# Optimization experiments

Measured on AMD Instinct MI355X. Metric: run time of the kernel, lower is better.

The kernel has to match this reference:

```python
import jax, jax.numpy as jnp
import numpy as np

IN_F, OUT_F = 64, 32
N = IN_F * OUT_F + OUT_F  # 2080 sampled parameters (weights + bias)
B, S = 8, 2048
SCALE_INIT = 1.0 * float(np.sqrt(2.0 / (IN_F + OUT_F)))


def setup_inputs() -> dict:
    key = jax.random.key(0)
    k_x, k_eps, k_loc, k_cov = jax.random.split(key, 4)
    x = jax.random.normal(k_x, (B, S, IN_F), dtype=jnp.float32)
    eps = jax.random.normal(k_eps, (B, S, N), dtype=jnp.float32)
    loc = 0.01 * jax.random.normal(k_loc, (N,), dtype=jnp.float32)
    logvar = jnp.full((N,), float(np.log(SCALE_INIT)), dtype=jnp.float32)
    n_off = N * (N - 1) // 2
    cov_flat = 0.001 * jax.random.normal(k_cov, (n_off,), dtype=jnp.float32)
    return {"x": x, "eps": eps, "loc": loc, "logvar": logvar, "cov_flat": cov_flat}


def reference(x, eps, loc, logvar, cov_flat):
    n = loc.shape[0]
    in_f = x.shape[-1]
    out_f = n // (in_f + 1)  # n = out*(in+1)
    # flat_to_triangular (strictly lower) + make_cholesky, vectorized scatter
    rows, cols = np.tril_indices(n, -1)
    A = jnp.zeros((n, n), dtype=x.dtype).at[rows, cols].set(cov_flat)
    L = A + jnp.diag(jnp.exp(logvar * 0.5))  # off-diag from cov, diag = std
    # MultivariateNormal rsample: loc + L @ eps (per batch sample)
    W = loc + jnp.einsum('bsn,mn->bsm', eps, L)  # [B,S,N]
    b = W[..., :out_f]
    Wm = W[..., out_f:].reshape(*W.shape[:-1], in_f, out_f)  # [B,S,in,out]
    y = jnp.einsum('bsh,bshk->bsk', x, Wm) + b
    return y
```

## Files before the change

### kernel.cpp

```cpp
#include <hip/hip_runtime.h>
#include <hip/hip_bf16.h>

#define IN_F  64
#define OUT_F 32
#define NV    2080
#define NPAD  2176
#define MM    16384
#define KK    2080
#define NBN   17

typedef __attribute__((ext_vector_type(4))) float f32x4;
typedef __bf16 bf16x8 __attribute__((ext_vector_type(8)));

using gas_ptr = const __attribute__((address_space(1))) void*;
using lds_ptr = __attribute__((address_space(3))) void*;

__global__ __launch_bounds__(256) void build_L_k(const float* __restrict__ cov,
                                                 const float* __restrict__ logvar,
                                                 __hip_bfloat16* __restrict__ LB) {
    const int idx = blockIdx.x * 256 + threadIdx.x;
    const int m = idx / KK;
    const int k = idx - m * KK;
    float v = 0.0f;
    if (m < NV) {
        if (k < m)       v = cov[(size_t)(m * (m - 1) / 2) + k];
        else if (k == m) v = expf(0.5f * logvar[m]);
    }
    LB[idx] = __float2bfloat16(v);
}

__global__ __launch_bounds__(256) void gemm_zl_k(const float* __restrict__ A,
                                                 const __hip_bfloat16* __restrict__ BT,
                                                 const float* __restrict__ loc,
                                                 const float* __restrict__ x,
                                                 float* __restrict__ Ypart) {
    __shared__ __align__(16) __hip_bfloat16 As[2][128 * 32];
    __shared__ __align__(16) __hip_bfloat16 Bs[2][128 * 32];
    __shared__ float xs[128][4];

    const int tid  = threadIdx.x;
    const int bm   = blockIdx.x;
    const int bn   = (NBN - 1) - blockIdx.y;
    const int wave = tid >> 6;
    const int lane = tid & 63;
    const int quad = lane >> 4;
    const int r16  = lane & 15;

    const int kblocks = min(KK / 32, 4 * bn + 4);

    {
        const int tl = tid >> 1;
        const int cc = (tid & 1) * 2;
#pragma unroll
        for (int c = cc; c < cc + 2; c++) {
            const int h = 4 * bn - 1 + c;
            float w = 0.0f;
            if (bn == 0 && c == 0)          w = 1.0f;
            else if (h >= 0 && h < IN_F)    w = x[(size_t)(bm * 128 + tl) * IN_F + h];
            xs[tl][c] = w;
        }
    }

    const float*          Ag = A  + (size_t)bm * 128 * KK;
    const __hip_bfloat16* Bg = BT + (size_t)bn * 128 * KK;

    const int c0 = tid, c1 = tid + 256;
    const int ar0 = c0 >> 2, ap0 = (c0 & 3) ^ ((ar0 >> 1) & 3);
    const int ar1 = c1 >> 2, ap1 = (c1 & 3) ^ ((ar1 >> 1) & 3);
    const size_t gofs0 = (size_t)ar0 * KK + ap0 * 8;
    const size_t gofs1 = (size_t)ar1 * KK + ap1 * 8;

    f32x4 acc[2][8];
#pragma unroll
    for (int i = 0; i < 2; i++)
#pragma unroll
        for (int j = 0; j < 8; j++) acc[i][j] = f32x4{0.f, 0.f, 0.f, 0.f};

    int aofs[2], bofs[8];
#pragma unroll
    for (int i = 0; i < 2; i++) {
        const int arow = 32 * wave + 16 * i + r16;
        aofs[i] = arow * 32 + (quad ^ ((arow >> 1) & 3)) * 8;
    }
#pragma unroll
    for (int j = 0; j < 8; j++) {
        const int brow = 16 * j + r16;
        bofs[j] = brow * 32 + (quad ^ ((brow >> 1) & 3)) * 8;
    }

    {
        f32x4 ra0 = *(const f32x4*)(Ag + gofs0);
        f32x4 ra1 = *(const f32x4*)(Ag + gofs0 + 4);
        f32x4 ra2 = *(const f32x4*)(Ag + gofs1);
        f32x4 ra3 = *(const f32x4*)(Ag + gofs1 + 4);
        __builtin_amdgcn_global_load_lds((gas_ptr)(Bg + gofs0), (lds_ptr)(&Bs[0][0] + c0 * 8), 16, 0, 0);
        __builtin_amdgcn_global_load_lds((gas_ptr)(Bg + gofs1), (lds_ptr)(&Bs[0][0] + c1 * 8), 16, 0, 0);
        bf16x8 w0, w1;
#pragma unroll
        for (int q = 0; q < 4; q++) {
            w0[q] = (__bf16)ra0[q]; w0[4 + q] = (__bf16)ra1[q];
            w1[q] = (__bf16)ra2[q]; w1[4 + q] = (__bf16)ra3[q];
        }
        *(bf16x8*)(&As[0][0] + c0 * 8) = w0;
        *(bf16x8*)(&As[0][0] + c1 * 8) = w1;
    }

    for (int kb = 0; kb < kblocks; ++kb) {
        const int cur = kb & 1;
        __syncthreads();

        const bool pf = (kb + 1 < kblocks);
        f32x4 ra0, ra1, ra2, ra3;
        if (pf) {
            const size_t k0 = (size_t)(kb + 1) * 32;
            ra0 = *(const f32x4*)(Ag + k0 + gofs0);
            ra1 = *(const f32x4*)(Ag + k0 + gofs0 + 4);
            ra2 = *(const f32x4*)(Ag + k0 + gofs1);
            ra3 = *(const f32x4*)(Ag + k0 + gofs1 + 4);
            __builtin_amdgcn_global_load_lds((gas_ptr)(Bg + k0 + gofs0), (lds_ptr)(&Bs[cur ^ 1][0] + c0 * 8), 16, 0, 0);
            __builtin_amdgcn_global_load_lds((gas_ptr)(Bg + k0 + gofs1), (lds_ptr)(&Bs[cur ^ 1][0] + c1 * 8), 16, 0, 0);
        }

        bf16x8 af[2], bfr[8];
#pragma unroll
        for (int i = 0; i < 2; i++) af[i]  = *(const bf16x8*)(&As[cur][0] + aofs[i]);
#pragma unroll
        for (int j = 0; j < 8; j++) bfr[j] = *(const bf16x8*)(&Bs[cur][0] + bofs[j]);
#pragma unroll
        for (int i = 0; i < 2; i++)
#pragma unroll
            for (int j = 0; j < 8; j++)
                acc[i][j] = __builtin_amdgcn_mfma_f32_16x16x32_bf16(af[i], bfr[j], acc[i][j], 0, 0, 0);

        if (pf) {
            bf16x8 w0, w1;
#pragma unroll
            for (int q = 0; q < 4; q++) {
                w0[q] = (__bf16)ra0[q]; w0[4 + q] = (__bf16)ra1[q];
                w1[q] = (__bf16)ra2[q]; w1[4 + q] = (__bf16)ra3[q];
            }
            *(bf16x8*)(&As[cur ^ 1][0] + c0 * 8) = w0;
            *(bf16x8*)(&As[cur ^ 1][0] + c1 * 8) = w1;
        }
    }

    float locv[8];
#pragma unroll
    for (int j = 0; j < 8; j++) {
        const int col = bn * 128 + 16 * j + r16;
        locv[j] = (col < NV) ? loc[col] : 0.0f;
    }

    float* yp = Ypart + ((size_t)bn * MM + (size_t)bm * 128) * OUT_F;
#pragma unroll
    for (int i = 0; i < 2; i++) {
#pragma unroll
        for (int r = 0; r < 4; r++) {
            const int tl = 32 * wave + 16 * i + 4 * quad + r;
            float v0 = 0.0f, v1 = 0.0f;
#pragma unroll
            for (int c = 0; c < 4; c++) {
                const float w = xs[tl][c];
                v0 += w * (acc[i][2 * c][r]     + locv[2 * c]);
                v1 += w * (acc[i][2 * c + 1][r] + locv[2 * c + 1]);
            }
            yp[(size_t)tl * OUT_F + r16]      = v0;
            yp[(size_t)tl * OUT_F + 16 + r16] = v1;
        }
    }
}

__global__ __launch_bounds__(256) void reduce_y_k(const float4* __restrict__ yp,
                                                  float4* __restrict__ y) {
    const size_t i = (size_t)blockIdx.x * 256 + threadIdx.x;
    float4 s = yp[i];
#pragma unroll
    for (int b = 1; b < NBN; b++) {
        float4 v = yp[i + (size_t)b * (MM * OUT_F / 4)];
        s.x += v.x; s.y += v.y; s.z += v.z; s.w += v.w;
    }
    y[i] = s;
}

extern "C" void kernel_launch(void* const* d_in, const int* in_sizes, int n_in,
                              void* d_out, int out_size, void* d_ws, size_t ws_size,
                              hipStream_t stream) {
    const float* x      = (const float*)d_in[0];
    const float* eps    = (const float*)d_in[1];
    const float* loc    = (const float*)d_in[2];
    const float* logvar = (const float*)d_in[3];
    const float* cov    = (const float*)d_in[4];
    float* y = (float*)d_out;

    char* ws = (char*)d_ws;
    __hip_bfloat16* LB    = (__hip_bfloat16*)ws;
    float*          Ypart = (float*)(ws + (size_t)NPAD * KK * 2);

    build_L_k<<<(NPAD * KK) / 256, 256, 0, stream>>>(cov, logvar, LB);
    gemm_zl_k<<<dim3(MM / 128, NBN), 256, 0, stream>>>(eps, LB, loc, x, Ypart);
    reduce_y_k<<<(MM * OUT_F / 4) / 256, 256, 0, stream>>>((const float4*)Ypart, (float4*)y);
}
```

Measured before the change: 314.5 us.

## Pre-convert eps to bf16 and use triple-buffered async GEMM with 256-row tiles

A fused prep kernel converts eps to bf16 in workspace while also building L. The GEMM then streams both operands with direct global-to-LDS loads into a three-stage buffer, uses 256-row M tiles (each wave computes 4x8 MFMA tiles), and skips MFMAs on the zero upper-triangular part of L in the diagonal blocks. This removes the in-loop fp32-to-bf16 conversion and register staging of A and raises data reuse per tile. The cost is an extra full pass over eps (read fp32, write bf16, read again) plus more LDS and register use. The old path stays as a fallback when the workspace is too small.

```diff
diff --git a/kernel.cpp b/kernel.cpp
--- a/kernel.cpp
+++ b/kernel.cpp
@@ -8,12 +8,43 @@
 #define MM    16384
 #define KK    2080
 #define NBN   17
+#define BM    256
+
+#define CVT_BLKS 16640
+#define L_BLKS   17680
 
 typedef __attribute__((ext_vector_type(4))) float f32x4;
 typedef __bf16 bf16x8 __attribute__((ext_vector_type(8)));
 
 using gas_ptr = const __attribute__((address_space(1))) void*;
 using lds_ptr = __attribute__((address_space(3))) void*;
+
+__global__ __launch_bounds__(256) void prep_k(const float* __restrict__ eps,
+                                              const float* __restrict__ cov,
+                                              const float* __restrict__ logvar,
+                                              __hip_bfloat16* __restrict__ EB,
+                                              __hip_bfloat16* __restrict__ LB) {
+    const int b = blockIdx.x;
+    if (b < CVT_BLKS) {
+        const size_t i = ((size_t)b * 256 + threadIdx.x) * 8;
+        const f32x4 a0 = *(const f32x4*)(eps + i);
+        const f32x4 a1 = *(const f32x4*)(eps + i + 4);
+        bf16x8 w;
+#pragma unroll
+        for (int q = 0; q < 4; q++) { w[q] = (__bf16)a0[q]; w[4 + q] = (__bf16)a1[q]; }
+        *(bf16x8*)(EB + i) = w;
+    } else {
+        const int idx = (b - CVT_BLKS) * 256 + threadIdx.x;
+        const int m = idx / KK;
+        const int k = idx - m * KK;
+        float v = 0.0f;
+        if (m < NV) {
+            if (k < m)       v = cov[(size_t)(m * (m - 1) / 2) + k];
+            else if (k == m) v = expf(0.5f * logvar[m]);
+        }
+        LB[idx] = __float2bfloat16(v);
+    }
+}
 
 __global__ __launch_bounds__(256) void build_L_k(const float* __restrict__ cov,
                                                  const float* __restrict__ logvar,
@@ -29,6 +60,151 @@
     LB[idx] = __float2bfloat16(v);
 }
 
+__global__ __launch_bounds__(256, 2) void gemm_v2_k(const __hip_bfloat16* __restrict__ EB,
+                                                    const __hip_bfloat16* __restrict__ LBt,
+                                                    const float* __restrict__ loc,
+                                                    const float* __restrict__ x,
+                                                    float* __restrict__ Ypart) {
+    __shared__ __align__(16) __hip_bfloat16 As[3][BM * 32];
+    __shared__ __align__(16) __hip_bfloat16 Bs[3][128 * 32];
+    __shared__ float xs[BM][4];
+
+    const int tid  = threadIdx.x;
+    const int bm   = blockIdx.x;
+    const int bn   = (NBN - 1) - blockIdx.y;
+    const int wave = tid >> 6;
+    const int lane = tid & 63;
+    const int quad = lane >> 4;
+    const int r16  = lane & 15;
+    const int kblocks = min(KK / 32, 4 * bn + 4);
+
+    {
+        const int row = bm * BM + tid;
+#pragma unroll
+        for (int c = 0; c < 4; c++) {
+            const int h = 4 * bn - 1 + c;
+            float w = 0.0f;
+            if (bn == 0 && c == 0)       w = 1.0f;
+            else if (h >= 0 && h < IN_F) w = x[(size_t)row * IN_F + h];
+            xs[tid][c] = w;
+        }
+    }
+
+    const __hip_bfloat16* __restrict__ Ag = EB  + (size_t)bm * BM * KK;
+    const __hip_bfloat16* __restrict__ Bg = LBt + (size_t)bn * 128 * KK;
+
+    size_t agofs[4]; int aldso[4];
+#pragma unroll
+    for (int u = 0; u < 4; u++) {
+        const int c = tid + 256 * u;
+        const int r = c >> 2, p = (c & 3) ^ ((r >> 1) & 3);
+        agofs[u] = (size_t)r * KK + (size_t)(p * 8);
+        aldso[u] = c * 8;
+    }
+    size_t bgofs[2]; int bldso[2];
+#pragma unroll
+    for (int u = 0; u < 2; u++) {
+        const int c = tid + 256 * u;
+        const int r = c >> 2, p = (c & 3) ^ ((r >> 1) & 3);
+        bgofs[u] = (size_t)r * KK + (size_t)(p * 8);
+        bldso[u] = c * 8;
+    }
+
+    int aofs[4], bofs[8];
+#pragma unroll
+    for (int i = 0; i < 4; i++) {
+        const int arow = 64 * wave + 16 * i + r16;
+        aofs[i] = arow * 32 + (quad ^ ((arow >> 1) & 3)) * 8;
+    }
+#pragma unroll
+    for (int j = 0; j < 8; j++) {
+        const int brow = 16 * j + r16;
+        bofs[j] = brow * 32 + (quad ^ ((brow >> 1) & 3)) * 8;
+    }
+
+    f32x4 acc[4][8];
+#pragma unroll
+    for (int i = 0; i < 4; i++)
+#pragma unroll
+        for (int j = 0; j < 8; j++) acc[i][j] = f32x4{0.f, 0.f, 0.f, 0.f};
+
+    auto stage = [&](int t, int buf) __attribute__((always_inline)) {
+        const size_t k0 = (size_t)t * 32;
+#pragma unroll
+        for (int u = 0; u < 4; u++)
+            __builtin_amdgcn_global_load_lds((gas_ptr)(Ag + k0 + agofs[u]),
+                                             (lds_ptr)(&As[buf][0] + aldso[u]), 16, 0, 0);
+#pragma unroll
+        for (int u = 0; u < 2; u++)
+            __builtin_amdgcn_global_load_lds((gas_ptr)(Bg + k0 + bgofs[u]),
+                                             (lds_ptr)(&Bs[buf][0] + bldso[u]), 16, 0, 0);
+    };
+
+    stage(0, 0);
+    stage(1, 1);
+    asm volatile("s_waitcnt lgkmcnt(0)" ::: "memory");
+    asm volatile("s_waitcnt vmcnt(6)" ::: "memory");
+    __builtin_amdgcn_s_barrier();
+    __builtin_amdgcn_sched_barrier(0);
+
+    auto iter = [&](int t, int jlo) __attribute__((always_inline)) {
+        if (t + 2 < kblocks) stage(t + 2, (t + 2) % 3);
+        const __hip_bfloat16* as = &As[t % 3][0];
+        const __hip_bfloat16* bs = &Bs[t % 3][0];
+        bf16x8 af[4], bfr[8];
+#pragma unroll
+        for (int i = 0; i < 4; i++) af[i] = *(const bf16x8*)(as + aofs[i]);
+#pragma unroll
+        for (int j = 0; j < 8; j++)
+            if (j >= jlo) bfr[j] = *(const bf16x8*)(bs + bofs[j]);
+#pragma unroll
+        for (int j = 0; j < 8; j++)
+            if (j >= jlo)
+#pragma unroll
+                for (int i = 0; i < 4; i++)
+                    acc[i][j] = __builtin_amdgcn_mfma_f32_16x16x32_bf16(af[i], bfr[j], acc[i][j], 0, 0, 0);
+        if (t + 2 < kblocks) {
+            asm volatile("s_waitcnt vmcnt(6)" ::: "memory");
+            __builtin_amdgcn_s_barrier();
+            __builtin_amdgcn_sched_barrier(0);
+        } else if (t + 1 < kblocks) {
+            asm volatile("s_waitcnt vmcnt(0)" ::: "memory");
+            __builtin_amdgcn_s_barrier();
+            __builtin_amdgcn_sched_barrier(0);
+        }
+    };
+
+    const int t_full = min(kblocks, 4 * bn + 1);
+    int t = 0;
+    for (; t < t_full; ++t) iter(t, 0);
+    for (; t < kblocks; ++t) iter(t, 2 * t - 8 * bn);
+
+    float locv[8];
+#pragma unroll
+    for (int j = 0; j < 8; j++) {
+        const int col = bn * 128 + 16 * j + r16;
+        locv[j] = (col < NV) ? loc[col] : 0.0f;
+    }
+
+    float* yp = Ypart + ((size_t)bn * MM + (size_t)bm * BM) * OUT_F;
+#pragma unroll
+    for (int i = 0; i < 4; i++) {
+#pragma unroll
+        for (int r = 0; r < 4; r++) {
+            const int tl = 64 * wave + 16 * i + 4 * quad + r;
+            float v0 = 0.0f, v1 = 0.0f;
+#pragma unroll
+            for (int c = 0; c < 4; c++) {
+                const float w = xs[tl][c];
+                v0 += w * (acc[i][2 * c][r]     + locv[2 * c]);
+                v1 += w * (acc[i][2 * c + 1][r] + locv[2 * c + 1]);
+            }
+            yp[(size_t)tl * OUT_F + r16]      = v0;
+            yp[(size_t)tl * OUT_F + 16 + r16] = v1;
+        }
+    }
+}
+
 __global__ __launch_bounds__(256) void gemm_zl_k(const float* __restrict__ A,
                                                  const __hip_bfloat16* __restrict__ BT,
                                                  const float* __restrict__ loc,
@@ -193,10 +369,24 @@
     float* y = (float*)d_out;
 
     char* ws = (char*)d_ws;
-    __hip_bfloat16* LB    = (__hip_bfloat16*)ws;
-    float*          Ypart = (float*)(ws + (size_t)NPAD * KK * 2);
-
-    build_L_k<<<(NPAD * KK) / 256, 256, 0, stream>>>(cov, logvar, LB);
-    gemm_zl_k<<<dim3(MM / 128, NBN), 256, 0, stream>>>(eps, LB, loc, x, Ypart);
-    reduce_y_k<<<(MM * OUT_F / 4) / 256, 256, 0, stream>>>((const float4*)Ypart, (float4*)y);
-}
+    const size_t lb_bytes = (size_t)NPAD * KK * 2;
+    const size_t eb_bytes = (size_t)MM * KK * 2;
+    const size_t yp_bytes = (size_t)NBN * MM * OUT_F * 4;
+
+    if (ws_size >= lb_bytes + eb_bytes + yp_bytes) {
+        __hip_bfloat16* LB    = (__hip_bfloat16*)ws;
+        __hip_bfloat16* EB    = (__hip_bfloat16*)(ws + lb_bytes);
+        float*          Ypart = (float*)(ws + lb_bytes + eb_bytes);
+
+        prep_k<<<CVT_BLKS + L_BLKS, 256, 0, stream>>>(eps, cov, logvar, EB, LB);
+        gemm_v2_k<<<dim3(MM / BM, NBN), 256, 0, stream>>>(EB, LB, loc, x, Ypart);
+        reduce_y_k<<<(MM * OUT_F / 4) / 256, 256, 0, stream>>>((const float4*)Ypart, (float4*)y);
+    } else {
+        __hip_bfloat16* LB    = (__hip_bfloat16*)ws;
+        float*          Ypart = (float*)(ws + lb_bytes);
+
+        build_L_k<<<(NPAD * KK) / 256, 256, 0, stream>>>(cov, logvar, LB);
+        gemm_zl_k<<<dim3(MM / 128, NBN), 256, 0, stream>>>(eps, LB, loc, x, Ypart);
+        reduce_y_k<<<(MM * OUT_F / 4) / 256, 256, 0, stream>>>((const float4*)Ypart, (float4*)y);
+    }
+}
```

Measured after the change: 325.4 us. +3.4%, slower.

## Enlarge GEMM M-tile to 256, triple-buffer B, skip zero triangular MFMAs

Applied to the files above, without the earlier changes.

The GEMM tile grows from 128 to 256 rows per block, so each B (L-transposed) tile loaded into LDS is reused across twice as many eps rows. B staging becomes a three-stage async pipeline with explicit waitcnt and barrier control, plus MFMA priority raising. In the diagonal k-blocks, MFMAs for column fragments whose L entries are all zero (upper triangle) are skipped. The larger tile halves the grid and raises register pressure (acc is now 4x8 f32x4), which could reduce occupancy despite the launch_bounds hint.

```diff
diff --git a/kernel.cpp b/kernel.cpp
--- a/kernel.cpp
+++ b/kernel.cpp
@@ -8,6 +8,7 @@
 #define MM    16384
 #define KK    2080
 #define NBN   17
+#define BM    256
 
 typedef __attribute__((ext_vector_type(4))) float f32x4;
 typedef __bf16 bf16x8 __attribute__((ext_vector_type(8)));
@@ -29,14 +30,14 @@
     LB[idx] = __float2bfloat16(v);
 }
 
-__global__ __launch_bounds__(256) void gemm_zl_k(const float* __restrict__ A,
-                                                 const __hip_bfloat16* __restrict__ BT,
-                                                 const float* __restrict__ loc,
-                                                 const float* __restrict__ x,
-                                                 float* __restrict__ Ypart) {
-    __shared__ __align__(16) __hip_bfloat16 As[2][128 * 32];
-    __shared__ __align__(16) __hip_bfloat16 Bs[2][128 * 32];
-    __shared__ float xs[128][4];
+__global__ __launch_bounds__(256, 2) void gemm_v3_k(const float* __restrict__ A,
+                                                    const __hip_bfloat16* __restrict__ BT,
+                                                    const float* __restrict__ loc,
+                                                    const float* __restrict__ x,
+                                                    float* __restrict__ Ypart) {
+    __shared__ __align__(16) __hip_bfloat16 As[2][BM * 32];
+    __shared__ __align__(16) __hip_bfloat16 Bs[3][128 * 32];
+    __shared__ float xs[BM][4];
 
     const int tid  = threadIdx.x;
     const int bm   = blockIdx.x;
@@ -45,41 +46,44 @@
     const int lane = tid & 63;
     const int quad = lane >> 4;
     const int r16  = lane & 15;
-
     const int kblocks = min(KK / 32, 4 * bn + 4);
 
     {
-        const int tl = tid >> 1;
-        const int cc = (tid & 1) * 2;
-#pragma unroll
-        for (int c = cc; c < cc + 2; c++) {
+        const int row = bm * BM + tid;
+#pragma unroll
+        for (int c = 0; c < 4; c++) {
             const int h = 4 * bn - 1 + c;
             float w = 0.0f;
-            if (bn == 0 && c == 0)          w = 1.0f;
-            else if (h >= 0 && h < IN_F)    w = x[(size_t)(bm * 128 + tl) * IN_F + h];
-            xs[tl][c] = w;
-        }
-    }
-
-    const float*          Ag = A  + (size_t)bm * 128 * KK;
-    const __hip_bfloat16* Bg = BT + (size_t)bn * 128 * KK;
-
-    const int c0 = tid, c1 = tid + 256;
-    const int ar0 = c0 >> 2, ap0 = (c0 & 3) ^ ((ar0 >> 1) & 3);
-    const int ar1 = c1 >> 2, ap1 = (c1 & 3) ^ ((ar1 >> 1) & 3);
-    const size_t gofs0 = (size_t)ar0 * KK + ap0 * 8;
-    const size_t gofs1 = (size_t)ar1 * KK + ap1 * 8;
-
-    f32x4 acc[2][8];
-#pragma unroll
-    for (int i = 0; i < 2; i++)
-#pragma unroll
-        for (int j = 0; j < 8; j++) acc[i][j] = f32x4{0.f, 0.f, 0.f, 0.f};
-
-    int aofs[2], bofs[8];
-#pragma unroll
-    for (int i = 0; i < 2; i++) {
-        const int arow = 32 * wave + 16 * i + r16;
+            if (bn == 0 && c == 0)       w = 1.0f;
+            else if (h >= 0 && h < IN_F) w = x[(size_t)row * IN_F + h];
+            xs[tid][c] = w;
+        }
+    }
+
+    const float*          __restrict__ Ag = A  + (size_t)bm * BM * KK;
+    const __hip_bfloat16* __restrict__ Bg = BT + (size_t)bn * 128 * KK;
+
+    size_t agofs[4]; int aldso[4];
+#pragma unroll
+    for (int u = 0; u < 4; u++) {
+        const int c = tid + 256 * u;
+        const int r = c >> 2, p = (c & 3) ^ ((r >> 1) & 3);
+        agofs[u] = (size_t)r * KK + (size_t)(p * 8);
+        aldso[u] = c * 8;
+    }
+    size_t bgofs[2]; int bldso[2];
+#pragma unroll
+    for (int u = 0; u < 2; u++) {
+        const int c = tid + 256 * u;
+        const int r = c >> 2, p = (c & 3) ^ ((r >> 1) & 3);
+        bgofs[u] = (size_t)r * KK + (size_t)(p * 8);
+        bldso[u] = c * 8;
+    }
+
+    int aofs[4], bofs[8];
+#pragma unroll
+    for (int i = 0; i < 4; i++) {
+        const int arow = 64 * wave + 16 * i + r16;
         aofs[i] = arow * 32 + (quad ^ ((arow >> 1) & 3)) * 8;
     }
 #pragma unroll
@@ -88,61 +92,90 @@
         bofs[j] = brow * 32 + (quad ^ ((brow >> 1) & 3)) * 8;
     }
 
-    {
-        f32x4 ra0 = *(const f32x4*)(Ag + gofs0);
-        f32x4 ra1 = *(const f32x4*)(Ag + gofs0 + 4);
-        f32x4 ra2 = *(const f32x4*)(Ag + gofs1);
-        f32x4 ra3 = *(const f32x4*)(Ag + gofs1 + 4);
-        __builtin_amdgcn_global_load_lds((gas_ptr)(Bg + gofs0), (lds_ptr)(&Bs[0][0] + c0 * 8), 16, 0, 0);
-        __builtin_amdgcn_global_load_lds((gas_ptr)(Bg + gofs1), (lds_ptr)(&Bs[0][0] + c1 * 8), 16, 0, 0);
-        bf16x8 w0, w1;
-#pragma unroll
-        for (int q = 0; q < 4; q++) {
-            w0[q] = (__bf16)ra0[q]; w0[4 + q] = (__bf16)ra1[q];
-            w1[q] = (__bf16)ra2[q]; w1[4 + q] = (__bf16)ra3[q];
-        }
-        *(bf16x8*)(&As[0][0] + c0 * 8) = w0;
-        *(bf16x8*)(&As[0][0] + c1 * 8) = w1;
-    }
-
-    for (int kb = 0; kb < kblocks; ++kb) {
-        const int cur = kb & 1;
-        __syncthreads();
-
-        const bool pf = (kb + 1 < kblocks);
-        f32x4 ra0, ra1, ra2, ra3;
-        if (pf) {
-            const size_t k0 = (size_t)(kb + 1) * 32;
-            ra0 = *(const f32x4*)(Ag + k0 + gofs0);
-            ra1 = *(const f32x4*)(Ag + k0 + gofs0 + 4);
-            ra2 = *(const f32x4*)(Ag + k0 + gofs1);
-            ra3 = *(const f32x4*)(Ag + k0 + gofs1 + 4);
-            __builtin_amdgcn_global_load_lds((gas_ptr)(Bg + k0 + gofs0), (lds_ptr)(&Bs[cur ^ 1][0] + c0 * 8), 16, 0, 0);
-            __builtin_amdgcn_global_load_lds((gas_ptr)(Bg + k0 + gofs1), (lds_ptr)(&Bs[cur ^ 1][0] + c1 * 8), 16, 0, 0);
-        }
-
-        bf16x8 af[2], bfr[8];
-#pragma unroll
-        for (int i = 0; i < 2; i++) af[i]  = *(const bf16x8*)(&As[cur][0] + aofs[i]);
-#pragma unroll
-        for (int j = 0; j < 8; j++) bfr[j] = *(const bf16x8*)(&Bs[cur][0] + bofs[j]);
-#pragma unroll
-        for (int i = 0; i < 2; i++)
-#pragma unroll
-            for (int j = 0; j < 8; j++)
-                acc[i][j] = __builtin_amdgcn_mfma_f32_16x16x32_bf16(af[i], bfr[j], acc[i][j], 0, 0, 0);
-
-        if (pf) {
-            bf16x8 w0, w1;
+    f32x4 acc[4][8];
+#pragma unroll
+    for (int i = 0; i < 4; i++)
+#pragma unroll
+        for (int j = 0; j < 8; j++) acc[i][j] = f32x4{0.f, 0.f, 0.f, 0.f};
+
+    f32x4 ra[8];
+
+    auto loadA = [&](int t) __attribute__((always_inline)) {
+        const size_t k0 = (size_t)t * 32;
+#pragma unroll
+        for (int u = 0; u < 4; u++) {
+            ra[2 * u]     = *(const f32x4*)(Ag + k0 + agofs[u]);
+            ra[2 * u + 1] = *(const f32x4*)(Ag + k0 + agofs[u] + 4);
+        }
+    };
+    auto writeA = [&](int buf) __attribute__((always_inline)) {
+#pragma unroll
+        for (int u = 0; u < 4; u++) {
+            bf16x8 w;
 #pragma unroll
             for (int q = 0; q < 4; q++) {
-                w0[q] = (__bf16)ra0[q]; w0[4 + q] = (__bf16)ra1[q];
-                w1[q] = (__bf16)ra2[q]; w1[4 + q] = (__bf16)ra3[q];
+                w[q]     = (__bf16)ra[2 * u][q];
+                w[4 + q] = (__bf16)ra[2 * u + 1][q];
             }
-            *(bf16x8*)(&As[cur ^ 1][0] + c0 * 8) = w0;
-            *(bf16x8*)(&As[cur ^ 1][0] + c1 * 8) = w1;
-        }
-    }
+            *(bf16x8*)(&As[buf][0] + aldso[u]) = w;
+        }
+    };
+    auto stageB = [&](int t, int buf) __attribute__((always_inline)) {
+        const size_t k0 = (size_t)t * 32;
+#pragma unroll
+        for (int u = 0; u < 2; u++)
+            __builtin_amdgcn_global_load_lds((gas_ptr)(Bg + k0 + bgofs[u]),
+                                             (lds_ptr)(&Bs[buf][0] + bldso[u]), 16, 0, 0);
+    };
+
+    loadA(0);
+    __builtin_amdgcn_sched_barrier(0);
+    stageB(0, 0);
+    stageB(1, 1);
+    __builtin_amdgcn_sched_barrier(0);
+    writeA(0);
+    loadA(1);
+    __builtin_amdgcn_sched_barrier(0);
+    asm volatile("s_waitcnt vmcnt(10)" ::: "memory");
+    asm volatile("s_waitcnt lgkmcnt(0)" ::: "memory");
+    __builtin_amdgcn_s_barrier();
+    __builtin_amdgcn_sched_barrier(0);
+
+    auto iter = [&](int t, int jlo) __attribute__((always_inline)) {
+        const bool pfA = (t + 1 < kblocks);
+        const bool pfB = (t + 2 < kblocks);
+        if (pfB) stageB(t + 2, (t + 2) % 3);
+        const __hip_bfloat16* as = &As[t & 1][0];
+        const __hip_bfloat16* bs = &Bs[t % 3][0];
+        bf16x8 af[4];
+#pragma unroll
+        for (int i = 0; i < 4; i++) af[i] = *(const bf16x8*)(as + aofs[i]);
+        __builtin_amdgcn_s_setprio(1);
+#pragma unroll
+        for (int j = 0; j < 8; j++) {
+            if (j >= jlo) {
+                const bf16x8 bf = *(const bf16x8*)(bs + bofs[j]);
+#pragma unroll
+                for (int i = 0; i < 4; i++)
+                    acc[i][j] = __builtin_amdgcn_mfma_f32_16x16x32_bf16(af[i], bf, acc[i][j], 0, 0, 0);
+            }
+        }
+        __builtin_amdgcn_s_setprio(0);
+        if (pfA) {
+            if (pfB) { asm volatile("s_waitcnt vmcnt(2)" ::: "memory"); }
+            else     { asm volatile("s_waitcnt vmcnt(0)" ::: "memory"); }
+            writeA((t + 1) & 1);
+            if (pfB) loadA(t + 2);
+            asm volatile("s_waitcnt lgkmcnt(0)" ::: "memory");
+            __builtin_amdgcn_s_barrier();
+            __builtin_amdgcn_sched_barrier(0);
+        }
+    };
+
+    const int t_full = min(kblocks, 4 * bn + 1);
+    int t = 0;
+    for (; t < t_full; ++t) iter(t, 0);
+    for (; t < kblocks; ++t) iter(t, 2 * t - 8 * bn);
 
     float locv[8];
 #pragma unroll
@@ -151,12 +184,12 @@
         locv[j] = (col < NV) ? loc[col] : 0.0f;
     }
 
-    float* yp = Ypart + ((size_t)bn * MM + (size_t)bm * 128) * OUT_F;
-#pragma unroll
-    for (int i = 0; i < 2; i++) {
+    float* yp = Ypart + ((size_t)bn * MM + (size_t)bm * BM) * OUT_F;
+#pragma unroll
+    for (int i = 0; i < 4; i++) {
 #pragma unroll
         for (int r = 0; r < 4; r++) {
-            const int tl = 32 * wave + 16 * i + 4 * quad + r;
+            const int tl = 64 * wave + 16 * i + 4 * quad + r;
             float v0 = 0.0f, v1 = 0.0f;
 #pragma unroll
             for (int c = 0; c < 4; c++) {
@@ -193,10 +226,11 @@
     float* y = (float*)d_out;
 
     char* ws = (char*)d_ws;
+    const size_t lb_bytes = (size_t)NPAD * KK * 2;
     __hip_bfloat16* LB    = (__hip_bfloat16*)ws;
-    float*          Ypart = (float*)(ws + (size_t)NPAD * KK * 2);
+    float*          Ypart = (float*)(ws + lb_bytes);
 
     build_L_k<<<(NPAD * KK) / 256, 256, 0, stream>>>(cov, logvar, LB);
-    gemm_zl_k<<<dim3(MM / 128, NBN), 256, 0, stream>>>(eps, LB, loc, x, Ypart);
+    gemm_v3_k<<<dim3(MM / BM, NBN), 256, 0, stream>>>(eps, LB, loc, x, Ypart);
     reduce_y_k<<<(MM * OUT_F / 4) / 256, 256, 0, stream>>>((const float4*)Ypart, (float4*)y);
 }
```

Result: no change. 315.6 us (+0.3%).
